# Kernel optimization log

Measured on AMD Instinct MI355X. Metric: run time of the kernel, lower is better.

The kernel has to match this reference:

```python
import jax, jax.numpy as jnp
import numpy as np

G = 128          # voxel grid side
R = 2048         # rays
S = 128          # samples per ray
VD = 28          # 1 density + 27 SH coeffs (3 channels x 9)

# SH constants (match source module)
Y00 = 0.5 * np.sqrt(1.0 / np.pi)
H3 = 0.5 * np.sqrt(3.0 / np.pi)
H15 = 0.5 * np.sqrt(15.0 / np.pi)
Q5 = 0.25 * np.sqrt(5.0 / np.pi)
Q15 = 0.25 * np.sqrt(15.0 / np.pi)


def setup_inputs() -> dict:
    key = jax.random.key(0)
    k1, k2, k3, k4 = jax.random.split(key, 4)
    grid = jax.random.uniform(k1, (G, G, G, VD), dtype=jnp.float32)
    # continuous positions strictly inside the grid so all 8 corners are valid
    sample_positions = jax.random.uniform(k2, (R, S, 3), dtype=jnp.float32) * (G - 2)
    sample_distances = jax.random.uniform(k3, (R, S), dtype=jnp.float32) * 0.05
    ang = jax.random.uniform(k4, (R, 2), dtype=jnp.float32)
    viewing_angles = ang * jnp.array([np.pi, 2.0 * np.pi], dtype=jnp.float32)
    return {"grid": grid, "sample_positions": sample_positions,
            "sample_distances": sample_distances, "viewing_angles": viewing_angles}


def sh_basis(viewing_angles):
    # order matches harmonic(): [C00, Cm11, C01, C11, Cm22, Cm12, C02, C12, C22]
    th, ph = viewing_angles[:, 0], viewing_angles[:, 1]
    st, ct = jnp.sin(th), jnp.cos(th)
    sp, cp = jnp.sin(ph), jnp.cos(ph)
    return jnp.stack([
        jnp.full_like(th, Y00),          # Y_0_0
        H3 * st * sp,                    # Y_m1_1
        H3 * ct,                         # Y_0_1
        H3 * st * cp,                    # Y_1_1
        H15 * st * cp * st * sp,         # Y_m2_2
        H15 * st * sp * ct,              # Y_m1_2
        Q5 * (3.0 * ct * ct - 1.0),      # Y_0_2
        H15 * st * cp * ct,              # Y_1_2
        Q15 * ((st * cp) ** 2 - (st * sp) ** 2),  # Y_2_2
    ], axis=-1)  # [R, 9]


def trilinear(grid, pos):
    # pos: [R, S, 3] continuous coords -> [R, S, VD]
    p0 = jnp.floor(pos).astype(jnp.int32)
    fd = pos - p0.astype(pos.dtype)                  # fractional offsets (x_d, y_d, z_d)
    gmax = jnp.int32(grid.shape[0] - 1)
    out = jnp.zeros(pos.shape[:-1] + (grid.shape[-1],), dtype=grid.dtype)
    for dx in (0, 1):
        wx = fd[..., 0] if dx else (1.0 - fd[..., 0])
        for dy in (0, 1):
            wy = fd[..., 1] if dy else (1.0 - fd[..., 1])
            for dz in (0, 1):
                wz = fd[..., 2] if dz else (1.0 - fd[..., 2])
                ix = jnp.clip(p0[..., 0] + dx, 0, gmax)
                iy = jnp.clip(p0[..., 1] + dy, 0, gmax)
                iz = jnp.clip(p0[..., 2] + dz, 0, gmax)
                out = out + (wx * wy * wz)[..., None] * grid[ix, iy, iz]
    return out


def reference(grid, sample_positions, sample_distances, viewing_angles):
    feats = trilinear(grid, sample_positions)          # [R, S, 28]
    sigma = feats[..., 0]                              # [R, S]
    coeffs = feats[..., 1:].reshape(feats.shape[0], feats.shape[1], 3, 9)
    att = jnp.exp(-sigma * sample_distances)           # exp(-sigma_j * d_j)
    # Faithful to source: transmittance[i] = sum_{j<=i} exp(-sigma_j d_j)
    trans = jnp.cumsum(att, axis=1)                    # inclusive cumsum
    weight = trans * (1.0 - att)                       # [R, S]
    Y = sh_basis(viewing_angles)                       # [R, 9]
    rgb = jnp.einsum('rscn,rn->rsc', coeffs, Y)        # [R, S, 3]
    return jnp.sum(weight[..., None] * rgb, axis=1)    # [R, 3]
```

## Files before the change

### kernel.cpp

```cpp
#include <hip/hip_runtime.h>

#define GDIM 128
#define NS   128
#define VD   28

__global__ __launch_bounds__(128) void plenoxel_kernel(
    const float* __restrict__ grid,
    const float* __restrict__ pos,
    const float* __restrict__ dist,
    const float* __restrict__ ang,
    float* __restrict__ out)
{
    const int r = blockIdx.x;
    const int s = threadIdx.x;
    const int lane = s & 63;

    const float th = ang[2 * r + 0];
    const float ph = ang[2 * r + 1];
    float st, ct, sp, cp;
    sincosf(th, &st, &ct);
    sincosf(ph, &sp, &cp);
    const float Y00 = 0.28209479177387814f;
    const float H3  = 0.4886025119029199f;
    const float H15 = 1.0925484305920792f;
    const float Q5  = 0.31539156525252005f;
    const float Q15 = 0.5462742152960396f;
    float Y[9];
    Y[0] = Y00;
    Y[1] = H3 * st * sp;
    Y[2] = H3 * ct;
    Y[3] = H3 * st * cp;
    Y[4] = H15 * (st * cp) * (st * sp);
    Y[5] = H15 * (st * sp) * ct;
    Y[6] = Q5 * (3.f * ct * ct - 1.f);
    Y[7] = H15 * (st * cp) * ct;
    Y[8] = Q15 * ((st * cp) * (st * cp) - (st * sp) * (st * sp));

    const float* p = pos + ((size_t)r * NS + s) * 3;
    const float x = p[0], y = p[1], z = p[2];
    const float fx0 = floorf(x), fy0 = floorf(y), fz0 = floorf(z);
    const int ix0 = (int)fx0, iy0 = (int)fy0, iz0 = (int)fz0;
    const float fx = x - fx0, fy = y - fy0, fz = z - fz0;

    int ix[2], iy[2], iz[2];
    ix[0] = min(max(ix0,     0), GDIM - 1);
    ix[1] = min(max(ix0 + 1, 0), GDIM - 1);
    iy[0] = min(max(iy0,     0), GDIM - 1);
    iy[1] = min(max(iy0 + 1, 0), GDIM - 1);
    iz[0] = min(max(iz0,     0), GDIM - 1);
    iz[1] = min(max(iz0 + 1, 0), GDIM - 1);
    const float wx[2] = {1.f - fx, fx};
    const float wy[2] = {1.f - fy, fy};
    const float wz[2] = {1.f - fz, fz};

    float sigma = 0.f, r0 = 0.f, r1 = 0.f, r2 = 0.f;
#pragma unroll
    for (int dx = 0; dx < 2; ++dx) {
#pragma unroll
        for (int dy = 0; dy < 2; ++dy) {
#pragma unroll
            for (int dz = 0; dz < 2; ++dz) {
                const float w = wx[dx] * wy[dy] * wz[dz];
                const size_t base =
                    (((size_t)ix[dx] * GDIM + iy[dy]) * GDIM + iz[dz]) * VD;
                const float4* g4 = (const float4*)(grid + base);
                float f[28];
#pragma unroll
                for (int j = 0; j < 7; ++j) ((float4*)f)[j] = g4[j];
                sigma += w * f[0];
                float a0 = 0.f, a1 = 0.f, a2 = 0.f;
#pragma unroll
                for (int n = 0; n < 9; ++n) {
                    a0 += f[1 + n]  * Y[n];
                    a1 += f[10 + n] * Y[n];
                    a2 += f[19 + n] * Y[n];
                }
                r0 += w * a0;
                r1 += w * a1;
                r2 += w * a2;
            }
        }
    }

    const float d = dist[(size_t)r * NS + s];
    const float att = expf(-sigma * d);

    float t = att;
#pragma unroll
    for (int o = 1; o < 64; o <<= 1) {
        const float v = __shfl_up(t, (unsigned)o, 64);
        if (lane >= o) t += v;
    }
    __shared__ float wave0_total;
    if (s == 63) wave0_total = t;
    __syncthreads();
    const float trans = t + (s >= 64 ? wave0_total : 0.f);
    const float weight = trans * (1.f - att);

    float w0 = weight * r0, w1 = weight * r1, w2 = weight * r2;
#pragma unroll
    for (int o = 32; o > 0; o >>= 1) {
        w0 += __shfl_down(w0, (unsigned)o, 64);
        w1 += __shfl_down(w1, (unsigned)o, 64);
        w2 += __shfl_down(w2, (unsigned)o, 64);
    }
    __shared__ float part[2][3];
    if (lane == 0) {
        const int wv = s >> 6;
        part[wv][0] = w0; part[wv][1] = w1; part[wv][2] = w2;
    }
    __syncthreads();
    if (s == 0) {
        out[(size_t)r * 3 + 0] = part[0][0] + part[1][0];
        out[(size_t)r * 3 + 1] = part[0][1] + part[1][1];
        out[(size_t)r * 3 + 2] = part[0][2] + part[1][2];
    }
}

extern "C" void kernel_launch(void* const* d_in, const int* in_sizes, int n_in,
                              void* d_out, int out_size, void* d_ws, size_t ws_size,
                              hipStream_t stream) {
    const float* grid = (const float*)d_in[0];
    const float* pos  = (const float*)d_in[1];
    const float* dst  = (const float*)d_in[2];
    const float* ang  = (const float*)d_in[3];
    float* out = (float*)d_out;

    const int R = in_sizes[3] / 2;
    plenoxel_kernel<<<R, NS, 0, stream>>>(grid, pos, dst, ang, out);
}
```

Measured before the change: 338.3 us.

## Split trilinear corner gathers across four thread groups per ray

Each block now uses 512 threads, so four threads handle each sample. Each thread gathers the two z-corners of one (dx,dy) pair and computes their partial density and SH colour. The partials are combined through shared memory before the scan and reduction. This exposes more memory-level parallelism for the random 112-byte grid gathers. The cost is duplicated position and SH setup work, an extra barrier and shared-memory traffic, and the final scan running on only a quarter of the threads.

```diff
diff --git a/kernel.cpp b/kernel.cpp
--- a/kernel.cpp
+++ b/kernel.cpp
@@ -4,16 +4,20 @@
 #define NS   128
 #define VD   28
 
-__global__ __launch_bounds__(128) void plenoxel_kernel(
+__global__ __launch_bounds__(512, 4) void plenoxel_kernel(
     const float* __restrict__ grid,
     const float* __restrict__ pos,
     const float* __restrict__ dist,
     const float* __restrict__ ang,
     float* __restrict__ out)
 {
-    const int r = blockIdx.x;
-    const int s = threadIdx.x;
-    const int lane = s & 63;
+    const int r   = blockIdx.x;
+    const int tid = threadIdx.x;
+    const int s   = tid & (NS - 1);
+    const int p   = tid >> 7;
+    const int dx  = p >> 1;
+    const int dy  = p & 1;
+    const int lane = tid & 63;
 
     const float th = ang[2 * r + 0];
     const float ph = ang[2 * r + 1];
@@ -36,84 +40,95 @@
     Y[7] = H15 * (st * cp) * ct;
     Y[8] = Q15 * ((st * cp) * (st * cp) - (st * sp) * (st * sp));
 
-    const float* p = pos + ((size_t)r * NS + s) * 3;
-    const float x = p[0], y = p[1], z = p[2];
+    const float* pp = pos + ((size_t)r * NS + s) * 3;
+    const float x = pp[0], y = pp[1], z = pp[2];
     const float fx0 = floorf(x), fy0 = floorf(y), fz0 = floorf(z);
-    const int ix0 = (int)fx0, iy0 = (int)fy0, iz0 = (int)fz0;
     const float fx = x - fx0, fy = y - fy0, fz = z - fz0;
+    const int jx  = min(max((int)fx0 + dx, 0), GDIM - 1);
+    const int jy  = min(max((int)fy0 + dy, 0), GDIM - 1);
+    const int jz0 = min(max((int)fz0,      0), GDIM - 1);
+    const int jz1 = min(max((int)fz0 + 1,  0), GDIM - 1);
 
-    int ix[2], iy[2], iz[2];
-    ix[0] = min(max(ix0,     0), GDIM - 1);
-    ix[1] = min(max(ix0 + 1, 0), GDIM - 1);
-    iy[0] = min(max(iy0,     0), GDIM - 1);
-    iy[1] = min(max(iy0 + 1, 0), GDIM - 1);
-    iz[0] = min(max(iz0,     0), GDIM - 1);
-    iz[1] = min(max(iz0 + 1, 0), GDIM - 1);
-    const float wx[2] = {1.f - fx, fx};
-    const float wy[2] = {1.f - fy, fy};
-    const float wz[2] = {1.f - fz, fz};
+    const float wxy = (dx ? fx : 1.f - fx) * (dy ? fy : 1.f - fy);
+    const float wz0 = wxy * (1.f - fz);
+    const float wz1 = wxy * fz;
 
-    float sigma = 0.f, r0 = 0.f, r1 = 0.f, r2 = 0.f;
+    const float4* g0 = (const float4*)(grid + (((size_t)jx * GDIM + jy) * GDIM + jz0) * VD);
+    const float4* g1 = (const float4*)(grid + (((size_t)jx * GDIM + jy) * GDIM + jz1) * VD);
+
+    float f0[28], f1[28];
 #pragma unroll
-    for (int dx = 0; dx < 2; ++dx) {
+    for (int j = 0; j < 7; ++j) ((float4*)f0)[j] = g0[j];
 #pragma unroll
-        for (int dy = 0; dy < 2; ++dy) {
+    for (int j = 0; j < 7; ++j) ((float4*)f1)[j] = g1[j];
+
+    float psig = wz0 * f0[0] + wz1 * f1[0];
+    float d0r = 0.f, d0g = 0.f, d0b = 0.f;
+    float d1r = 0.f, d1g = 0.f, d1b = 0.f;
 #pragma unroll
-            for (int dz = 0; dz < 2; ++dz) {
-                const float w = wx[dx] * wy[dy] * wz[dz];
-                const size_t base =
-                    (((size_t)ix[dx] * GDIM + iy[dy]) * GDIM + iz[dz]) * VD;
-                const float4* g4 = (const float4*)(grid + base);
-                float f[28];
+    for (int n = 0; n < 9; ++n) {
+        d0r += f0[1 + n]  * Y[n];
+        d0g += f0[10 + n] * Y[n];
+        d0b += f0[19 + n] * Y[n];
+        d1r += f1[1 + n]  * Y[n];
+        d1g += f1[10 + n] * Y[n];
+        d1b += f1[19 + n] * Y[n];
+    }
+    const float pr = wz0 * d0r + wz1 * d1r;
+    const float pg = wz0 * d0g + wz1 * d1g;
+    const float pb = wz0 * d0b + wz1 * d1b;
+
+    __shared__ float4 part[512];
+    part[tid] = make_float4(psig, pr, pg, pb);
+    __syncthreads();
+
+    __shared__ float wave0_total;
+    __shared__ float fin[2][3];
+
+    float t = 0.f, att = 0.f, rr = 0.f, rg = 0.f, rb = 0.f;
+    if (tid < NS) {
+        const float4 a = part[s];
+        const float4 b = part[s + 128];
+        const float4 c = part[s + 256];
+        const float4 e = part[s + 384];
+        const float sigma = a.x + b.x + c.x + e.x;
+        rr = a.y + b.y + c.y + e.y;
+        rg = a.z + b.z + c.z + e.z;
+        rb = a.w + b.w + c.w + e.w;
+
+        const float d = dist[(size_t)r * NS + s];
+        att = expf(-sigma * d);
+
+        t = att;
 #pragma unroll
-                for (int j = 0; j < 7; ++j) ((float4*)f)[j] = g4[j];
-                sigma += w * f[0];
-                float a0 = 0.f, a1 = 0.f, a2 = 0.f;
+        for (int o = 1; o < 64; o <<= 1) {
+            const float v = __shfl_up(t, (unsigned)o, 64);
+            if (lane >= o) t += v;
+        }
+        if (tid == 63) wave0_total = t;
+    }
+    __syncthreads();
+
+    if (tid < NS) {
+        const float trans  = t + (tid >= 64 ? wave0_total : 0.f);
+        const float weight = trans * (1.f - att);
+        float a0 = weight * rr, a1 = weight * rg, a2 = weight * rb;
 #pragma unroll
-                for (int n = 0; n < 9; ++n) {
-                    a0 += f[1 + n]  * Y[n];
-                    a1 += f[10 + n] * Y[n];
-                    a2 += f[19 + n] * Y[n];
-                }
-                r0 += w * a0;
-                r1 += w * a1;
-                r2 += w * a2;
-            }
+        for (int o = 32; o > 0; o >>= 1) {
+            a0 += __shfl_down(a0, (unsigned)o, 64);
+            a1 += __shfl_down(a1, (unsigned)o, 64);
+            a2 += __shfl_down(a2, (unsigned)o, 64);
+        }
+        if (lane == 0) {
+            const int wv = tid >> 6;
+            fin[wv][0] = a0; fin[wv][1] = a1; fin[wv][2] = a2;
         }
     }
-
-    const float d = dist[(size_t)r * NS + s];
-    const float att = expf(-sigma * d);
-
-    float t = att;
-#pragma unroll
-    for (int o = 1; o < 64; o <<= 1) {
-        const float v = __shfl_up(t, (unsigned)o, 64);
-        if (lane >= o) t += v;
-    }
-    __shared__ float wave0_total;
-    if (s == 63) wave0_total = t;
     __syncthreads();
-    const float trans = t + (s >= 64 ? wave0_total : 0.f);
-    const float weight = trans * (1.f - att);
-
-    float w0 = weight * r0, w1 = weight * r1, w2 = weight * r2;
-#pragma unroll
-    for (int o = 32; o > 0; o >>= 1) {
-        w0 += __shfl_down(w0, (unsigned)o, 64);
-        w1 += __shfl_down(w1, (unsigned)o, 64);
-        w2 += __shfl_down(w2, (unsigned)o, 64);
-    }
-    __shared__ float part[2][3];
-    if (lane == 0) {
-        const int wv = s >> 6;
-        part[wv][0] = w0; part[wv][1] = w1; part[wv][2] = w2;
-    }
-    __syncthreads();
-    if (s == 0) {
-        out[(size_t)r * 3 + 0] = part[0][0] + part[1][0];
-        out[(size_t)r * 3 + 1] = part[0][1] + part[1][1];
-        out[(size_t)r * 3 + 2] = part[0][2] + part[1][2];
+    if (tid == 0) {
+        out[(size_t)r * 3 + 0] = fin[0][0] + fin[1][0];
+        out[(size_t)r * 3 + 1] = fin[0][1] + fin[1][1];
+        out[(size_t)r * 3 + 2] = fin[0][2] + fin[1][2];
     }
 }
 
@@ -127,5 +142,5 @@
     float* out = (float*)d_out;
 
     const int R = in_sizes[3] / 2;
-    plenoxel_kernel<<<R, NS, 0, stream>>>(grid, pos, dst, ang, out);
+    plenoxel_kernel<<<R, 512, 0, stream>>>(grid, pos, dst, ang, out);
 }
```

New measurement: 370.3 us. 9.5% more time.
